# Kernel optimization log

Measured on AMD Instinct MI355X. Metric: run time of the kernel, lower is better.

## Reference

```python
import jax, jax.numpy as jnp
import numpy as np
from jax import lax

B = 2
IMG = 640.0
MIN_LEVEL, MAX_LEVEL = 3, 7
NUM_CLASSES = 91          # includes background (index 0)
MAX_TOTAL = 100
IOU_THR = 0.3
SCORE_THR = 0.05
PRE_NMS = 5000
BBOX_CLIP = float(np.log(1000.0 / 16.0))  # standard box-transform clip


def _level_anchors(level):
    """RetinaNet-style anchors for one pyramid level, [H*W*9, 4] in (y1,x1,y2,x2)."""
    stride = 2 ** level
    feat = int(IMG) // stride
    cy = (np.arange(feat, dtype=np.float32) + 0.5) * stride
    cx = (np.arange(feat, dtype=np.float32) + 0.5) * stride
    cy, cx = np.meshgrid(cy, cx, indexing='ij')
    base = 4.0 * stride
    anchors = []
    for octave in (2 ** 0.0, 2 ** (1.0 / 3.0), 2 ** (2.0 / 3.0)):
        for ar in (0.5, 1.0, 2.0):
            h = base * octave * np.sqrt(ar)
            w = base * octave / np.sqrt(ar)
            anchors.append(np.stack([cy - h / 2, cx - w / 2, cy + h / 2, cx + w / 2], -1))
    a = np.stack(anchors, -2).reshape(-1, 4)
    return a.astype(np.float32)


def setup_inputs():
    key = jax.random.key(0)
    inp = {}
    for level in range(MIN_LEVEL, MAX_LEVEL + 1):
        anc = _level_anchors(level)
        n = anc.shape[0]
        key, kb, kc = jax.random.split(key, 3)
        inp[f'box_outputs_{level}'] = 0.2 * jax.random.normal(kb, (B, n, 4), jnp.float32)
        inp[f'class_outputs_{level}'] = jax.random.normal(kc, (B, n, NUM_CLASSES), jnp.float32) - 2.0
        inp[f'anchor_boxes_{level}'] = jnp.broadcast_to(jnp.asarray(anc)[None], (B, n, 4))
    inp['image_shape'] = jnp.full((B, 2), IMG, jnp.float32)
    return inp


def _decode_boxes(enc, anchors):
    # faithful to box_utils.decode_boxes (with the +1/-1 pixel convention)
    dy, dx = enc[..., 0], enc[..., 1]
    dh = jnp.minimum(enc[..., 2], BBOX_CLIP)
    dw = jnp.minimum(enc[..., 3], BBOX_CLIP)
    ah = anchors[..., 2] - anchors[..., 0] + 1.0
    aw = anchors[..., 3] - anchors[..., 1] + 1.0
    ayc = anchors[..., 0] + 0.5 * ah
    axc = anchors[..., 1] + 0.5 * aw
    yc = dy * ah + ayc
    xc = dx * aw + axc
    h = jnp.exp(dh) * ah
    w = jnp.exp(dw) * aw
    ymin = yc - 0.5 * h
    xmin = xc - 0.5 * w
    return jnp.stack([ymin, xmin, ymin + h - 1.0, xmin + w - 1.0], axis=-1)


def _clip_boxes(boxes, image_shape):
    h = image_shape[:, 0:1]
    w = image_shape[:, 1:2]
    max_len = jnp.stack([h, w, h, w], axis=-1)  # [B,1,4]
    return jnp.clip(boxes, 0.0, max_len)


def _greedy_nms(scores, boxes):
    """Sorted greedy NMS over one (batch, class) lane.
    scores: [K] sorted descending (filtered entries are -1), boxes: [K,4].
    Returns top MAX_TOTAL selected (score, box) in descending score order,
    padded with score=-1 / zero boxes (matches sorted_non_max_suppression_padded).
    """
    areas = (boxes[:, 2] - boxes[:, 0]) * (boxes[:, 3] - boxes[:, 1])

    def step(active, _):
        masked = jnp.where(active, scores, -jnp.inf)
        i = jnp.argmax(masked)
        s = masked[i]
        valid = s > -1.0
        b = boxes[i]
        yy1 = jnp.maximum(b[0], boxes[:, 0])
        xx1 = jnp.maximum(b[1], boxes[:, 1])
        yy2 = jnp.minimum(b[2], boxes[:, 2])
        xx2 = jnp.minimum(b[3], boxes[:, 3])
        inter = jnp.maximum(yy2 - yy1, 0.0) * jnp.maximum(xx2 - xx1, 0.0)
        iou = inter / ((b[2] - b[0]) * (b[3] - b[1]) + areas - inter + 1e-8)
        active = active & (iou <= IOU_THR)
        active = active.at[i].set(False)
        out_s = jnp.where(valid, s, -1.0)
        out_b = jnp.where(valid, b, jnp.zeros_like(b))
        return active, (out_s, out_b)

    _, (sel_s, sel_b) = lax.scan(step, jnp.ones(scores.shape[0], bool), None, length=MAX_TOTAL)
    return sel_s, sel_b


def reference(box_outputs_3, box_outputs_4, box_outputs_5, box_outputs_6, box_outputs_7,
              class_outputs_3, class_outputs_4, class_outputs_5, class_outputs_6, class_outputs_7,
              anchor_boxes_3, anchor_boxes_4, anchor_boxes_5, anchor_boxes_6, anchor_boxes_7,
              image_shape):
    box_list = [box_outputs_3, box_outputs_4, box_outputs_5, box_outputs_6, box_outputs_7]
    cls_list = [class_outputs_3, class_outputs_4, class_outputs_5, class_outputs_6, class_outputs_7]
    anc_list = [anchor_boxes_3, anchor_boxes_4, anchor_boxes_5, anchor_boxes_6, anchor_boxes_7]

    boxes, scores = [], []
    for bo, co, an in zip(box_list, cls_list, anc_list):
        scores.append(jax.nn.sigmoid(co)[..., 1:])            # drop background class 0
        boxes.append(_clip_boxes(_decode_boxes(bo, an), image_shape))
    boxes = jnp.concatenate(boxes, axis=1)                     # [B,N,4] class-agnostic
    scores = jnp.concatenate(scores, axis=1)                   # [B,N,C]

    scores_t = jnp.transpose(scores, (0, 2, 1))                # [B,C,N]
    k = min(scores_t.shape[-1], PRE_NMS)
    top_s, idx = lax.top_k(scores_t, k)                        # [B,C,K]
    top_b = jax.vmap(lambda b, i: b[i])(boxes, idx)            # [B,C,K,4]

    # filter_boxes_by_scores: score -> -1, boxes -> 0 below threshold
    mask = top_s >= SCORE_THR
    top_s = jnp.where(mask, top_s, -1.0)
    top_b = top_b * mask[..., None].astype(top_b.dtype)

    sel_s, sel_b = jax.vmap(jax.vmap(_greedy_nms))(top_s, top_b)  # [B,C,T], [B,C,T,4]
    Bsz, C, T = sel_s.shape
    classes = jnp.broadcast_to(jnp.arange(C, dtype=jnp.int32)[None, :, None], (Bsz, C, T))

    flat_s = sel_s.reshape(Bsz, C * T)
    flat_b = sel_b.reshape(Bsz, C * T, 4)
    flat_c = classes.reshape(Bsz, C * T)

    final_s, fidx = lax.top_k(flat_s, MAX_TOTAL)
    final_b = jnp.take_along_axis(flat_b, fidx[..., None], axis=1)
    final_c = jnp.take_along_axis(flat_c, fidx, axis=1) + 1    # nmsed_classes += 1
    valid = jnp.sum((final_s > -1.0).astype(jnp.int32), axis=1)
    return final_b, final_s, final_c, valid
```

## Files before the change

kernel.cpp:

```cpp
#include <hip/hip_runtime.h>
#include <hip/hip_bf16.h>

typedef unsigned long long u64;
typedef unsigned int u32;

#define A_TOTAL 76725
#define NCLS 90
#define KTOP 5000u
#define MAXT 100
#define KTHR 0x3D4CCCCDu
#define TCAP 2048u
#define SCAP 512u
#define NSEL 384u

__device__ __forceinline__ u64 pack_key(u32 k, u32 i) {
  return ((u64)k << 32) | (u64)(0xFFFFFFFFu - i);
}

__device__ __forceinline__ int dig05(u64 k) {
  float s = __uint_as_float((u32)(k >> 32));
  int d = (int)((s - 0.5f) * 8175.0f);
  return min(max(d, 0), 4095);
}

__device__ __forceinline__ void cut4096w(const u32* hh, u32 need, int wl,
                                         u32& B, u32& incl, u32& above, u32& total) {
  int lo = wl << 6;
  u32 s = 0;
  #pragma unroll
  for (int j = 0; j < 64; ++j) s += hh[lo + j];
  u32 suf = s;
  #pragma unroll
  for (int off = 1; off < 64; off <<= 1) {
    u32 v = __shfl_down(suf, off, 64);
    if (wl < 64 - off) suf += v;
  }
  total = __shfl(suf, 0, 64);
  if (total < need) { B = 0; incl = total; above = 0; return; }
  u32 sufnext = suf - s;
  bool cross = (suf >= need) && (sufnext < need);
  u64 bal = __ballot(cross);
  int gl = (int)__ffsll((unsigned long long)bal) - 1;
  int glo = gl << 6;
  u32 aboveG = __shfl(sufnext, gl, 64);
  u32 hb = hh[glo + wl];
  u32 sufb = hb;
  #pragma unroll
  for (int off = 1; off < 64; off <<= 1) {
    u32 v = __shfl_down(sufb, off, 64);
    if (wl < 64 - off) sufb += v;
  }
  bool c2 = (aboveG + sufb >= need) && (aboveG + sufb - hb < need);
  u64 bal2 = __ballot(c2);
  int jB = (int)__ffsll((unsigned long long)bal2) - 1;
  B = (u32)(glo + jB);
  incl = aboveG + __shfl(sufb, jB, 64);
  above = incl - __shfl(hb, jB, 64);
}

__device__ __forceinline__ void bitonic_desc(u64* a, u32 n, int tid, int nth) {
  u32 P = 2; while (P < n) P <<= 1;
  for (u32 i = tid; i < P; i += nth) if (i >= n) a[i] = 0ULL;
  __syncthreads();
  for (u32 kk = 2; kk <= P; kk <<= 1) {
    for (u32 jj = kk >> 1; jj; jj >>= 1) {
      for (u32 i = tid; i < P; i += nth) {
        u32 ixj = i ^ jj;
        if (ixj > i) {
          u64 x = a[i], y = a[ixj];
          bool up = ((i & kk) == 0);
          if (up ? (x < y) : (x > y)) { a[i] = y; a[ixj] = x; }
        }
      }
      __syncthreads();
    }
  }
}

__device__ __forceinline__ int lazy_scan_g(const u64* key_s, const float4* boxes4, size_t bbase,
                                           int C, float4* wbox, float* outS, float* outB,
                                           int w, int wl) {
  int cur = 0;
  while (w < MAXT && cur < C) {
    int p = cur + wl;
    bool alive = (p < C);
    u64 kk = alive ? key_s[p] : 0ull;
    float4 mybox = make_float4(0.f, 0.f, 0.f, 0.f);
    if (alive) {
      u32 idx = 0xFFFFFFFFu - (u32)(kk & 0xFFFFFFFFull);
      mybox = boxes4[bbase + idx];
    }
    float myarea = alive ? (mybox.z - mybox.x) * (mybox.w - mybox.y) : 0.f;
    for (int j = 0; j < w; ++j) {
      if (alive) {
        float4 pb = wbox[j];
        float yy1 = fmaxf(pb.x, mybox.x), xx1 = fmaxf(pb.y, mybox.y);
        float yy2 = fminf(pb.z, mybox.z), xx2 = fminf(pb.w, mybox.w);
        float inter = fmaxf(yy2 - yy1, 0.0f) * fmaxf(xx2 - xx1, 0.0f);
        if (inter > 0.0f) {
          float pa = (pb.z - pb.x) * (pb.w - pb.y);
          if (inter / (pa + myarea - inter + 1e-8f) > 0.3f) alive = false;
        }
      }
    }
    for (;;) {
      u64 bal = __ballot(alive);
      if (bal == 0ull) break;
      int js = (int)__ffsll((unsigned long long)bal) - 1;
      float4 pb;
      pb.x = __shfl(mybox.x, js, 64);
      pb.y = __shfl(mybox.y, js, 64);
      pb.z = __shfl(mybox.z, js, 64);
      pb.w = __shfl(mybox.w, js, 64);
      u64 wk = __shfl(kk, js, 64);
      if (wl == 0) {
        outS[w] = __uint_as_float((u32)(wk >> 32));
        *(float4*)(outB + w * 4) = pb;
        wbox[w] = pb;
      }
      w++;
      if (w >= MAXT) break;
      if (wl <= js) alive = false;
      else if (alive) {
        float yy1 = fmaxf(pb.x, mybox.x), xx1 = fmaxf(pb.y, mybox.y);
        float yy2 = fminf(pb.z, mybox.z), xx2 = fminf(pb.w, mybox.w);
        float inter = fmaxf(yy2 - yy1, 0.0f) * fmaxf(xx2 - xx1, 0.0f);
        if (inter > 0.0f) {
          float pa = (pb.z - pb.x) * (pb.w - pb.y);
          if (inter / (pa + myarea - inter + 1e-8f) > 0.3f) alive = false;
        }
      }
    }
    cur += 64;
  }
  return w;
}

__device__ __forceinline__ void coll_elem(int i, float x, int b, int base, int slice,
                                          u64* __restrict__ listT_g, u32* __restrict__ cnt_pad) {
  if (x >= 0.0f) {
    u32 a = (u32)i / 91u;
    u32 c = (u32)i - a * 91u;
    if (c != 0u) {
      float s = 1.0f / (1.0f + expf(-x));
      int lane = b * NCLS + (int)c - 1;
      u32 idx = (u32)base + a;
      u32 p = atomicAdd(&cnt_pad[lane * 128 + slice * 16], 1u);
      if (p < SCAP) listT_g[(((size_t)lane * 8 + slice) << 9) + p] = pack_key(__float_as_uint(s), idx);
    }
  }
}

__global__ __launch_bounds__(256) void front_kernel(
    const float* __restrict__ bx0, const float* __restrict__ bx1, const float* __restrict__ bx2,
    const float* __restrict__ bx3, const float* __restrict__ bx4,
    const float* __restrict__ an0, const float* __restrict__ an1, const float* __restrict__ an2,
    const float* __restrict__ an3, const float* __restrict__ an4,
    const float* __restrict__ c3, const float* __restrict__ c4, const float* __restrict__ c5,
    const float* __restrict__ c6, const float* __restrict__ c7,
    const float* __restrict__ img, float* __restrict__ boxes,
    u64* __restrict__ listT_g, u32* __restrict__ cnt_pad)
{
  int blk = blockIdx.x, tid = threadIdx.x;
  if (blk < 600) {
    int t = blk * 256 + tid;
    if (t >= 2 * A_TOTAL) return;
    int b = t / A_TOTAL, a = t % A_TOTAL;
    const float* bp; const float* ap; int al; int nl;
    if (a < 57600)      { bp = bx0; ap = an0; al = a;          nl = 57600; }
    else if (a < 72000) { bp = bx1; ap = an1; al = a - 57600;  nl = 14400; }
    else if (a < 75600) { bp = bx2; ap = an2; al = a - 72000;  nl = 3600;  }
    else if (a < 76500) { bp = bx3; ap = an3; al = a - 75600;  nl = 900;   }
    else                { bp = bx4; ap = an4; al = a - 76500;  nl = 225;   }
    float4 e  = *(const float4*)(bp + ((size_t)b * nl + al) * 4);
    float4 an = *(const float4*)(ap + ((size_t)b * nl + al) * 4);
    const float CLIP = 4.135166556742356f;
    float ah  = an.z - an.x + 1.0f;
    float aw  = an.w - an.y + 1.0f;
    float ayc = an.x + 0.5f * ah;
    float axc = an.y + 0.5f * aw;
    float dh = fminf(e.z, CLIP), dw = fminf(e.w, CLIP);
    float yc = e.x * ah + ayc;
    float xc = e.y * aw + axc;
    float h  = expf(dh) * ah;
    float w  = expf(dw) * aw;
    float ymin = yc - 0.5f * h;
    float xmin = xc - 0.5f * w;
    float ymax = ymin + h - 1.0f;
    float xmax = xmin + w - 1.0f;
    float H = img[b * 2 + 0], W = img[b * 2 + 1];
    float4 o;
    o.x = fminf(fmaxf(ymin, 0.0f), H);
    o.y = fminf(fmaxf(xmin, 0.0f), W);
    o.z = fminf(fmaxf(ymax, 0.0f), H);
    o.w = fminf(fmaxf(xmax, 0.0f), W);
    *(float4*)(boxes + (size_t)t * 4) = o;
    return;
  }
  int blk2 = blk - 600;
  int slice = blk2 & 7;
  const float* cls; int n, base, b, loc, J, lvl;
  if (blk2 < 2560)      { lvl = 0; cls = c3; n = 57600; base = 0;     J = 1280; int r = blk2;        b = r >= J; loc = b ? r - J : r; }
  else if (blk2 < 3200) { lvl = 1; cls = c4; n = 14400; base = 57600; J = 320;  int r = blk2 - 2560; b = r >= J; loc = b ? r - J : r; }
  else if (blk2 < 3360) { lvl = 2; cls = c5; n = 3600;  base = 72000; J = 80;   int r = blk2 - 3200; b = r >= J; loc = b ? r - J : r; }
  else if (blk2 < 3400) { lvl = 3; cls = c6; n = 900;   base = 75600; J = 20;   int r = blk2 - 3360; b = r >= J; loc = b ? r - J : r; }
  else                  { lvl = 4; cls = c7; n = 225;   base = 76500; J = 10;   int r = blk2 - 3400; b = r >= J; loc = b ? r - J : r; }

  if (lvl <= 3) {
    int F4 = n * 91 / 4;
    int chunk = (F4 + J - 1) / J;
    int q0 = loc * chunk;
    int q1 = q0 + chunk; if (q1 > F4) q1 = F4;
    const float4* src4 = (const float4*)(cls + (size_t)b * n * 91);
    for (int q = q0 + tid; q < q1; q += 256) {
      float4 v = src4[q];
      int i0 = q << 2;
      coll_elem(i0,     v.x, b, base, slice, listT_g, cnt_pad);
      coll_elem(i0 + 1, v.y, b, base, slice, listT_g, cnt_pad);
      coll_elem(i0 + 2, v.z, b, base, slice, listT_g, cnt_pad);
      coll_elem(i0 + 3, v.w, b, base, slice, listT_g, cnt_pad);
    }
  } else {
    int F = n * 91;
    int chunk = (F + J - 1) / J;
    int s0 = loc * chunk;
    int s1 = s0 + chunk; if (s1 > F) s1 = F;
    const float* src = cls + (size_t)b * F;
    for (int i = s0 + tid; i < s1; i += 256) coll_elem(i, src[i], b, base, slice, listT_g, cnt_pad);
  }
}

__global__ __launch_bounds__(256) void nms_kernel(
    const float* __restrict__ c3, const float* __restrict__ c4, const float* __restrict__ c5,
    const float* __restrict__ c6, const float* __restrict__ c7,
    const float* __restrict__ boxes, const u64* __restrict__ listT_g,
    const u32* __restrict__ cnt_pad, float* __restrict__ nms_s, float* __restrict__ nms_b)
{
  __shared__ __align__(16) char big[40960];
  __shared__ __align__(16) u64 listE[2048];
  __shared__ u64 key_s[2048];
  __shared__ __align__(16) u32 histL[4096];
  __shared__ float4 wbox[MAXT];
  __shared__ u32 wtot[4];
  __shared__ u32 sh_flag, sh_mid, sh_bigS, sh_cS;
  __shared__ u64 sh_minPrev;
  __shared__ u32 sh_w, sh_done, sh_eidx, sh_Rthr, sh_eSorted, sh_bigF;
  __shared__ u32 sh_B, sh_incl, sh_above, sh_total, sh_cA, sh_cE, sh_B2;

  int tid = threadIdx.x;
  int lane = blockIdx.x;
  int b = lane / NCLS, c = lane % NCLS;
  const float4* boxes4 = (const float4*)boxes;
  size_t bbase = (size_t)b * A_TOTAL;
  const u64 thrpack = ((u64)KTHR) << 32;

  float* outS = nms_s + (size_t)lane * MAXT;
  float* outB = nms_b + (size_t)lane * MAXT * 4;

  u32 pre[9]; pre[0] = 0;
  bool of = false;
  #pragma unroll
  for (int j = 0; j < 8; ++j) {
    u32 cj = cnt_pad[lane * 128 + j * 16];
    of |= (cj > SCAP);
    pre[j + 1] = pre[j] + cj;
  }
  u32 cnt = pre[8];
  if (tid == 0) { sh_flag = (of || cnt > TCAP) ? 1u : 0u; sh_mid = 0; sh_bigS = 0; }
  __syncthreads();

  if (!sh_flag) {
    u64 kr[8];
    #pragma unroll
    for (int r = 0; r < 8; ++r) {
      u32 s = (u32)tid + (u32)r * 256u;
      u64 k = 0ull;
      if (s < cnt) {
        u32 j = 0;
        #pragma unroll
        for (int t = 1; t < 8; ++t) if (s >= pre[t]) j = (u32)t;
        k = listT_g[(((size_t)lane * 8 + j) << 9) + (s - pre[j])];
      }
      kr[r] = k;
    }

    for (int i = tid; i < 4096; i += 256) histL[i] = 0;
    __syncthreads();
    #pragma unroll
    for (int r = 0; r < 8; ++r) if (kr[r]) atomicAdd(&histL[dig05(kr[r])], 1u);
    __syncthreads();
    if (tid < 64) {
      u32 Bx, ix, ax, tx;
      cut4096w(histL, NSEL, tid, Bx, ix, ax, tx);
      if (tid == 0) { sh_B = Bx; sh_incl = ix; sh_total = tx; sh_cS = 0; }
    }
    __syncthreads();
    u32 B = sh_B, incl = sh_incl, total = sh_total;
    bool selAll = (total < NSEL);
    u32 Csel = selAll ? total : incl;
    if (Csel <= 768u) {
      u64* sel = (u64*)histL;
      #pragma unroll
      for (int r = 0; r < 8; ++r) {
        u64 k = kr[r];
        if (k && (selAll || (u32)dig05(k) >= B)) {
          u32 p = atomicAdd(&sh_cS, 1u);
          if (p < 768u) sel[p] = k;
        }
      }
      __syncthreads();
      u32 Cs = sh_cS; if (Cs > 768u) Cs = 768u;
      for (u32 j = tid; j < Cs; j += 256) {
        u64 kj = sel[j];
        u32 rk = 0;
        for (u32 i2 = 0; i2 < Cs; ++i2) rk += (sel[i2] > kj) ? 1u : 0u;
        key_s[rk] = kj;
      }
      __syncthreads();
      if (tid < 64) {
        int w = lazy_scan_g(key_s, boxes4, bbase, (int)Cs, wbox, outS, outB, 0, tid);
        if (tid == 0) {
          sh_w = (u32)w;
          if (w < MAXT) { if (selAll) sh_flag = 1; else sh_mid = 1; }
        }
      }
    } else {
      if (tid == 0) sh_mid = 1;
    }
    __syncthreads();

    if (sh_mid && !sh_flag) {
      for (int i = tid; i < 4096; i += 256) histL[i] = 0;
      if (tid == 0) sh_bigS = 0;
      __syncthreads();
      #pragma unroll
      for (int r = 0; r < 8; ++r) if (kr[r]) atomicAdd(&histL[dig05(kr[r])], 1u);
      __syncthreads();
      {
        int t0 = tid << 4;
        u32 hloc[16]; u32 ssum = 0;
        #pragma unroll
        for (int j = 0; j < 16; ++j) { hloc[j] = histL[t0 + j]; ssum += hloc[j]; }
        int wl = tid & 63, wid = tid >> 6;
        u32 suf = ssum;
        #pragma unroll
        for (int off = 1; off < 64; off <<= 1) {
          u32 v = __shfl_down(suf, off, 64);
          if (wl < 64 - off) suf += v;
        }
        if (wl == 0) wtot[wid] = suf;
        __syncthreads();
        u32 cross = 0;
        for (int w2 = wid + 1; w2 < 4; ++w2) cross += wtot[w2];
        u32 run = (suf - ssum) + cross;
        #pragma unroll
        for (int j = 15; j >= 0; --j) { u32 b2 = run; run += hloc[j]; histL[t0 + j] = b2; }
      }
      __syncthreads();
      #pragma unroll
      for (int r = 0; r < 8; ++r) {
        u64 k = kr[r];
        if (k) {
          u32 pos = atomicAdd(&histL[dig05(k)], 1u);
          if (pos < TCAP) key_s[pos] = k;
        }
      }
      __syncthreads();
      {
        int t0 = tid << 4;
        for (int j = 0; j < 16; ++j) {
          u32 d = (u32)(t0 + j);
          u32 end = histL[d];
          u32 start = (d == 4095u) ? 0u : histL[d + 1];
          u32 cc = end - start;
          if (cc >= 2u) {
            if (cc <= 48u) {
              for (u32 a2 = start + 1; a2 < end; ++a2) {
                u64 kv = key_s[a2];
                int bi = (int)a2 - 1;
                while (bi >= (int)start && key_s[bi] < kv) { key_s[bi + 1] = key_s[bi]; --bi; }
                key_s[bi + 1] = kv;
              }
            } else sh_bigS = 1;
          }
        }
      }
      __syncthreads();
      if (sh_bigS) bitonic_desc(key_s, cnt, tid, 256);
      if (tid < 64) {
        int w = lazy_scan_g(key_s, boxes4, bbase, (int)cnt, wbox, outS, outB, 0, tid);
        if (tid == 0) {
          sh_w = (u32)w;
          if (w < MAXT) sh_flag = 1;
        }
      }
    }
  }
  __syncthreads();
  if (!sh_flag) {
    u32 w = sh_w;
    for (u32 p = w + (u32)tid; p < MAXT; p += 256) {
      outS[p] = -1.0f;
      *(float4*)(outB + p * 4) = make_float4(0.f, 0.f, 0.f, 0.f);
    }
    return;
  }

  auto sb_of = [&](int i) -> u32 {
    const float* p; int al, nl;
    if (i < 57600)      { p = c3; al = i;          nl = 57600; }
    else if (i < 72000) { p = c4; al = i - 57600;  nl = 14400; }
    else if (i < 75600) { p = c5; al = i - 72000;  nl = 3600;  }
    else if (i < 76500) { p = c6; al = i - 75600;  nl = 900;   }
    else                { p = c7; al = i - 76500;  nl = 225;   }
    float x = p[((size_t)b * nl + al) * 91 + (c + 1)];
    float s = 1.0f / (1.0f + expf(-x));
    return __float_as_uint(s);
  };

  u64* listA = (u64*)big;
  for (int i = tid; i < 4096; i += 256) histL[i] = 0;
  if (tid == 0) {
    sh_cA = 0; sh_cE = 0; sh_w = 0; sh_done = 0; sh_eidx = 0; sh_eSorted = 0; sh_minPrev = ~0ull;
  }
  __syncthreads();
  for (int i = tid; i < A_TOTAL; i += 256) atomicAdd(&histL[sb_of(i) >> 19], 1u);
  __syncthreads();
  if (tid < 64) {
    u32 Bx, ix, ax, tx;
    cut4096w(histL, KTOP, tid, Bx, ix, ax, tx);
    if (tid == 0) sh_B = Bx;
  }
  __syncthreads();
  u32 B = sh_B;
  for (int i = tid; i < A_TOTAL; i += 256) {
    u32 u = sb_of(i);
    u32 bkt = u >> 19;
    if (bkt > B) {
      u32 p = atomicAdd(&sh_cA, 1u);
      if (p < 5120u) listA[p] = pack_key(u, (u32)i);
    } else if (bkt == B) {
      u32 p = atomicAdd(&sh_cE, 1u);
      if (p < 2048u) listE[p] = pack_key(u, (u32)i);
    }
  }
  __syncthreads();
  u32 g = sh_cA, h = sh_cE;
  if (h > 2048u) {
    for (int i = tid; i < 4096; i += 256) histL[i] = 0;
    if (tid == 0) sh_cE = 0;
    __syncthreads();
    for (int i = tid; i < A_TOTAL; i += 256) {
      u32 u = sb_of(i);
      if ((u >> 19) == B) atomicAdd(&histL[(u >> 7) & 0xFFFu], 1u);
    }
    __syncthreads();
    u32 R1 = KTOP - g;
    if (tid < 64) {
      u32 Bx, ix, ax, tx;
      cut4096w(histL, R1, tid, Bx, ix, ax, tx);
      if (tid == 0) sh_B2 = Bx;
    }
    __syncthreads();
    u32 B2 = sh_B2;
    for (int i = tid; i < A_TOTAL; i += 256) {
      u32 u = sb_of(i);
      if ((u >> 19) == B) {
        u32 sb2 = (u >> 7) & 0xFFFu;
        if (sb2 > B2) {
          u32 p = atomicAdd(&sh_cA, 1u);
          if (p < 5120u) listA[p] = pack_key(u, (u32)i);
        } else if (sb2 == B2) {
          u32 p = atomicAdd(&sh_cE, 1u);
          if (p < 2048u) listE[p] = pack_key(u, (u32)i);
        }
      }
    }
    __syncthreads();
    g = sh_cA; h = sh_cE; if (h > 2048u) h = 2048u;
  }
  if (g > 5120u) g = 5120u;
  u32 R = (g < KTOP) ? (KTOP - g) : 0u; if (R > h) R = h;

  u64 ak[20];
  #pragma unroll
  for (int r = 0; r < 20; ++r) {
    u32 s2 = (u32)tid + (u32)r * 256u;
    u64 kp = (s2 < g) ? listA[s2] : 0ull;
    if (kp < thrpack) kp = 0ull;
    ak[r] = kp;
  }
  __syncthreads();
  u32* cntArr = (u32*)big;

  const float LO0  = 0.04f;
  const float INV0 = 4096.0f / (1.001f - 0.04f);

  for (int seg = 0; seg < 7200; ++seg) {
    __syncthreads();
    if (sh_w >= MAXT || sh_done) break;
    u64 minPrev = sh_minPrev;

    int digLvl = 0;
    u32 A_B0 = 0, A_B1 = 0;
    float lo1 = 0.f, inv1 = 0.f;
    u64 kMask = 0, kPref = 0;
    int m1shift = 32;
    int selMode = -1;
    u32 selB = 0;
    u32 C = 0;
    bool fromE = false;

    for (int lvl = 0; lvl < 8; ++lvl) {
      for (int i = tid; i < 4096; i += 256) histL[i] = 0;
      __syncthreads();
      #pragma unroll
      for (int r = 0; r < 20; ++r) {
        u64 k = ak[r];
        if (!k || k >= minPrev) continue;
        float s = __uint_as_float((u32)(k >> 32));
        if (digLvl >= 1) { int d0 = (int)((s - LO0) * INV0); d0 = min(max(d0, 0), 4095); if ((u32)d0 != A_B0) continue; }
        if (digLvl >= 2) { int d1 = (int)((s - lo1) * inv1); d1 = min(max(d1, 0), 4095); if ((u32)d1 != A_B1) continue; }
        if (digLvl >= 3 && ((k & kMask) != kPref)) continue;
        u32 d;
        if (digLvl == 0)      { int t0 = (int)((s - LO0) * INV0); d = (u32)min(max(t0, 0), 4095); }
        else if (digLvl == 1) { int t1 = (int)((s - lo1) * inv1); d = (u32)min(max(t1, 0), 4095); }
        else                  d = (u32)((k >> m1shift) & 0xFFFull);
        atomicAdd(&histL[d], 1u);
      }
      __syncthreads();
      if (tid < 64) {
        u32 Bx, ix, ax, tx;
        cut4096w(histL, 1024u, tid, Bx, ix, ax, tx);
        if (tid == 0) { sh_B = Bx; sh_incl = ix; sh_above = ax; sh_total = tx; }
      }
      __syncthreads();
      u32 total = sh_total, incl = sh_incl, above = sh_above, Bx = sh_B;
      if (total == 0u)   { fromE = true; break; }
      if (total < 1024u) { selMode = 0; C = total; break; }
      if (incl <= 2048u) { selMode = 1; selB = Bx; C = incl; break; }
      if (above > 0u)    { selMode = 2; selB = Bx; C = above; break; }
      if (digLvl == 0) {
        A_B0 = Bx;
        lo1 = LO0 + (float)Bx / INV0;
        inv1 = INV0 * 4096.0f;
        digLvl = 1;
      } else if (digLvl == 1) {
        A_B1 = Bx;
        digLvl = 2; m1shift = 32;
      } else {
        kPref |= ((u64)Bx << m1shift);
        kMask |= (0xFFFull << m1shift);
        m1shift -= 12;
        digLvl++;
      }
      __syncthreads();
    }

    if (fromE) {
      if (!sh_eSorted) {
        bitonic_desc(listE, h, tid, 256);
        if (tid == 0) {
          u32 lo = 0, hi2 = h;
          while (lo < hi2) { u32 mid = (lo + hi2) >> 1; if (listE[mid] >= thrpack) lo = mid + 1; else hi2 = mid; }
          sh_Rthr = (R < lo) ? R : lo;
          sh_eSorted = 1;
        }
        __syncthreads();
      }
      u32 eidx = sh_eidx;
      u32 take = (sh_Rthr > eidx) ? (sh_Rthr - eidx) : 0u;
      if (take > 2048u) take = 2048u;
      if (take == 0u) { if (tid == 0) sh_done = 1; continue; }
      for (u32 i = tid; i < take; i += 256) key_s[i] = listE[eidx + i];
      C = take;
      if (tid == 0) sh_eidx = eidx + take;
    } else {
      u32 hloc[16];
      {
        int t0 = tid << 4;
        u32 ssum = 0;
        #pragma unroll
        for (int j = 0; j < 16; ++j) { hloc[j] = histL[t0 + j]; ssum += hloc[j]; }
        int wl = tid & 63, wid = tid >> 6;
        u32 suf = ssum;
        #pragma unroll
        for (int off = 1; off < 64; off <<= 1) {
          u32 v = __shfl_down(suf, off, 64);
          if (wl < 64 - off) suf += v;
        }
        if (wl == 0) wtot[wid] = suf;
        __syncthreads();
        u32 cross = 0;
        for (int w2 = wid + 1; w2 < 4; ++w2) cross += wtot[w2];
        u32 run = (suf - ssum) + cross;
        #pragma unroll
        for (int j = 15; j >= 0; --j) { u32 base2 = run; run += hloc[j]; histL[t0 + j] = base2; }
      }
      for (int i = tid; i < 4096; i += 256) cntArr[i] = 0;
      if (tid == 0) sh_bigF = 0;
      __syncthreads();
      #pragma unroll
      for (int r = 0; r < 20; ++r) {
        u64 k = ak[r];
        if (!k || k >= minPrev) continue;
        float s = __uint_as_float((u32)(k >> 32));
        if (digLvl >= 1) { int d0 = (int)((s - LO0) * INV0); d0 = min(max(d0, 0), 4095); if ((u32)d0 != A_B0) continue; }
        if (digLvl >= 2) { int d1 = (int)((s - lo1) * inv1); d1 = min(max(d1, 0), 4095); if ((u32)d1 != A_B1) continue; }
        if (digLvl >= 3 && ((k & kMask) != kPref)) continue;
        u32 d;
        if (digLvl == 0)      { int t0x = (int)((s - LO0) * INV0); d = (u32)min(max(t0x, 0), 4095); }
        else if (digLvl == 1) { int t1x = (int)((s - lo1) * inv1); d = (u32)min(max(t1x, 0), 4095); }
        else                  d = (u32)((k >> m1shift) & 0xFFFull);
        if (selMode == 1)      { if (d < selB) continue; }
        else if (selMode == 2) { if (d <= selB) continue; }
        u32 pos = histL[d] + atomicAdd(&cntArr[d], 1u);
        if (pos < 2048u) key_s[pos] = k;
      }
      __syncthreads();
      {
        int t0 = tid << 4;
        for (int j = 0; j < 16; ++j) {
          u32 bkt = (u32)(t0 + j);
          u32 cc = cntArr[bkt];
          if (cc >= 2u) {
            if (cc <= 48u) {
              u32 basep = histL[bkt];
              for (u32 a2 = 1; a2 < cc; ++a2) {
                u64 kv = key_s[basep + a2];
                int bi = (int)a2 - 1;
                while (bi >= 0 && key_s[basep + bi] < kv) { key_s[basep + bi + 1] = key_s[basep + bi]; --bi; }
                key_s[basep + bi + 1] = kv;
              }
            } else sh_bigF = 1;
          }
        }
      }
      __syncthreads();
      if (sh_bigF) bitonic_desc(key_s, C, tid, 256);
      if (tid == 0) sh_minPrev = key_s[C - 1];
    }
    __syncthreads();

    if (tid < 64) {
      int w = lazy_scan_g(key_s, boxes4, bbase, (int)C, wbox, outS, outB, (int)sh_w, tid);
      if (tid == 0) sh_w = (u32)w;
    }
  }

  __syncthreads();
  u32 w = sh_w;
  for (u32 p = w + (u32)tid; p < MAXT; p += 256) {
    outS[p] = -1.0f;
    *(float4*)(outB + p * 4) = make_float4(0.f, 0.f, 0.f, 0.f);
  }
}

__global__ __launch_bounds__(256) void merge_kernel(
    const float* __restrict__ nms_s, const float* __restrict__ nms_b,
    float* __restrict__ out_b, float* __restrict__ out_s,
    float* __restrict__ out_c, float* __restrict__ out_v)
{
  __shared__ u64 keys[NCLS * MAXT];
  __shared__ u32 hist[4096];
  __shared__ u64 sel[640];
  __shared__ u32 sh_cnt, sh_valid;
  __shared__ u32 sh_B, sh_incl, sh_above, sh_total;

  int b = blockIdx.x, tid = threadIdx.x;
  const int NTOT = NCLS * MAXT;

  for (int i = tid; i < NTOT; i += 256) {
    float s = nms_s[(size_t)b * NTOT + i];
    u32 u = __float_as_uint(s);
    u = (u & 0x80000000u) ? ~u : (u | 0x80000000u);
    keys[i] = ((u64)u << 32) | (u64)(0xFFFFFFFFu - (u32)i);
  }
  if (tid == 0) { sh_cnt = 0; sh_valid = 0; }

  u64 prefVal = 0;
  u64 T = 0;
  u32 need = MAXT;
  const int shifts[6] = {52, 40, 28, 16, 4, 0};
  const int widths[6] = {12, 12, 12, 12, 12, 4};
  for (int lvl = 0; lvl < 6; ++lvl) {
    int s = shifts[lvl], w = widths[lvl];
    for (int i = tid; i < 4096; i += 256) hist[i] = 0;
    __syncthreads();
    u32 dmask = (1u << w) - 1u;
    for (int i = tid; i < NTOT; i += 256) {
      u64 k = keys[i];
      if (lvl > 0 && (k >> (s + w)) != (prefVal >> (s + w))) continue;
      atomicAdd(&hist[(u32)((k >> s) & dmask)], 1u);
    }
    __syncthreads();
    if (tid < 64) {
      u32 Bx, ix, ax, tx;
      cut4096w(hist, need, tid, Bx, ix, ax, tx);
      if (tid == 0) { sh_B = Bx; sh_incl = ix; sh_above = ax; sh_total = tx; }
    }
    __syncthreads();
    u32 B = sh_B, incl = sh_incl, above = sh_above;
    if (incl <= 512u || lvl == 5) {
      T = prefVal | ((u64)B << s);
      break;
    }
    prefVal |= ((u64)B << s);
    need -= above;
  }
  __syncthreads();

  for (int i = tid; i < NTOT; i += 256) {
    u64 k = keys[i];
    if (k >= T) {
      u32 p = atomicAdd(&sh_cnt, 1u);
      if (p < 640u) sel[p] = k;
    }
  }
  __syncthreads();
  u32 cnt = sh_cnt; if (cnt > 640u) cnt = 640u;

  for (u32 j = tid; j < cnt; j += 256) {
    u64 kj = sel[j];
    u32 r = 0;
    for (u32 i = 0; i < cnt; ++i) r += (sel[i] > kj) ? 1u : 0u;
    if (r < (u32)MAXT) {
      u32 u = (u32)(kj >> 32);
      u32 bits = (u & 0x80000000u) ? (u ^ 0x80000000u) : ~u;
      float sc = __uint_as_float(bits);
      u32 flat = 0xFFFFFFFFu - (u32)(kj & 0xFFFFFFFFull);
      int cls = (int)(flat / MAXT), pos = (int)(flat % MAXT);
      out_s[b * MAXT + r] = sc;
      out_c[b * MAXT + r] = (float)(cls + 1);
      *(float4*)(out_b + ((size_t)b * MAXT + r) * 4) =
          *(const float4*)(nms_b + (((size_t)b * NCLS + cls) * MAXT + pos) * 4);
      if (sc > -1.0f) atomicAdd(&sh_valid, 1u);
    }
  }
  __syncthreads();
  if (tid == 0) out_v[b] = (float)sh_valid;
}

extern "C" void kernel_launch(void* const* d_in, const int* in_sizes, int n_in,
                              void* d_out, int out_size, void* d_ws, size_t ws_size,
                              hipStream_t stream)
{
  const float* box[5]; const float* cls[5]; const float* anc[5];
  bool interleaved = (in_sizes[1] == 2 * 57600 * 91);
  if (interleaved) {
    for (int l = 0; l < 5; ++l) {
      box[l] = (const float*)d_in[3 * l + 0];
      cls[l] = (const float*)d_in[3 * l + 1];
      anc[l] = (const float*)d_in[3 * l + 2];
    }
  } else {
    for (int l = 0; l < 5; ++l) {
      box[l] = (const float*)d_in[l];
      cls[l] = (const float*)d_in[5 + l];
      anc[l] = (const float*)d_in[10 + l];
    }
  }
  const float* img = (const float*)d_in[15];

  float* ws = (float*)d_ws;
  float* boxes_ws = ws;
  u32*   cnt_pad  = (u32*)(boxes_ws + 613800);
  u64*   listT_g  = (u64*)(cnt_pad + 180 * 128);
  float* nms_s    = (float*)(listT_g + 180 * 8 * 512);
  float* nms_b    = nms_s + 18000;

  hipMemsetAsync(cnt_pad, 0, 180 * 128 * sizeof(u32), stream);

  front_kernel<<<4020, 256, 0, stream>>>(
      box[0], box[1], box[2], box[3], box[4],
      anc[0], anc[1], anc[2], anc[3], anc[4],
      cls[0], cls[1], cls[2], cls[3], cls[4],
      img, boxes_ws, listT_g, cnt_pad);

  nms_kernel<<<180, 256, 0, stream>>>(cls[0], cls[1], cls[2], cls[3], cls[4],
                                      boxes_ws, listT_g, cnt_pad, nms_s, nms_b);

  float* out_b = (float*)d_out;
  float* out_s = out_b + 800;
  float* out_c = out_s + 200;
  float* out_v = out_c + 200;
  merge_kernel<<<2, 256, 0, stream>>>(nms_s, nms_b, out_b, out_s, out_c, out_v);
}
```

Measured before the change: 114.9 us.

## Split monolithic NMS kernel into sort, scan and fallback kernels

The single per-class NMS kernel is split into three launches. A 256-thread sort kernel does a full histogram-bucket sort of the candidate keys into global memory. A 64-thread scan kernel with small shared memory runs the lazy greedy NMS scan, and a fallback kernel handles only the classes flagged as overflowing or short. The partial top-384 selection path is dropped. The broadcast of the winning box now goes through shared memory instead of five shuffles. This is meant to cut the heavy shared-memory footprint and idle threads during the serial scan, at the cost of extra launches and a global round trip for the sorted keys.

```diff
diff --git a/kernel.cpp b/kernel.cpp
--- a/kernel.cpp
+++ b/kernel.cpp
@@ -11,7 +11,6 @@
 #define KTHR 0x3D4CCCCDu
 #define TCAP 2048u
 #define SCAP 512u
-#define NSEL 384u
 
 __device__ __forceinline__ u64 pack_key(u32 k, u32 i) {
   return ((u64)k << 32) | (u64)(0xFFFFFFFFu - i);
@@ -107,17 +106,12 @@
       u64 bal = __ballot(alive);
       if (bal == 0ull) break;
       int js = (int)__ffsll((unsigned long long)bal) - 1;
-      float4 pb;
-      pb.x = __shfl(mybox.x, js, 64);
-      pb.y = __shfl(mybox.y, js, 64);
-      pb.z = __shfl(mybox.z, js, 64);
-      pb.w = __shfl(mybox.w, js, 64);
-      u64 wk = __shfl(kk, js, 64);
-      if (wl == 0) {
-        outS[w] = __uint_as_float((u32)(wk >> 32));
-        *(float4*)(outB + w * 4) = pb;
-        wbox[w] = pb;
-      }
+      if (wl == js) {
+        wbox[w] = mybox;
+        outS[w] = __uint_as_float((u32)(kk >> 32));
+        *(float4*)(outB + w * 4) = mybox;
+      }
+      float4 pb = wbox[w];
       w++;
       if (w >= MAXT) break;
       if (wl <= js) alive = false;
@@ -230,32 +224,16 @@
   }
 }
 
-__global__ __launch_bounds__(256) void nms_kernel(
-    const float* __restrict__ c3, const float* __restrict__ c4, const float* __restrict__ c5,
-    const float* __restrict__ c6, const float* __restrict__ c7,
-    const float* __restrict__ boxes, const u64* __restrict__ listT_g,
-    const u32* __restrict__ cnt_pad, float* __restrict__ nms_s, float* __restrict__ nms_b)
+__global__ __launch_bounds__(256) void sort_kernel(
+    const u64* __restrict__ listT_g, const u32* __restrict__ cnt_pad,
+    u64* __restrict__ sortedK, u32* __restrict__ C_g, u32* __restrict__ flags)
 {
-  __shared__ __align__(16) char big[40960];
-  __shared__ __align__(16) u64 listE[2048];
+  __shared__ u32 histL[4096];
   __shared__ u64 key_s[2048];
-  __shared__ __align__(16) u32 histL[4096];
-  __shared__ float4 wbox[MAXT];
   __shared__ u32 wtot[4];
-  __shared__ u32 sh_flag, sh_mid, sh_bigS, sh_cS;
-  __shared__ u64 sh_minPrev;
-  __shared__ u32 sh_w, sh_done, sh_eidx, sh_Rthr, sh_eSorted, sh_bigF;
-  __shared__ u32 sh_B, sh_incl, sh_above, sh_total, sh_cA, sh_cE, sh_B2;
-
+  __shared__ u32 sh_big;
   int tid = threadIdx.x;
   int lane = blockIdx.x;
-  int b = lane / NCLS, c = lane % NCLS;
-  const float4* boxes4 = (const float4*)boxes;
-  size_t bbase = (size_t)b * A_TOTAL;
-  const u64 thrpack = ((u64)KTHR) << 32;
-
-  float* outS = nms_s + (size_t)lane * MAXT;
-  float* outB = nms_b + (size_t)lane * MAXT * 4;
 
   u32 pre[9]; pre[0] = 0;
   bool of = false;
@@ -266,145 +244,134 @@
     pre[j + 1] = pre[j] + cj;
   }
   u32 cnt = pre[8];
-  if (tid == 0) { sh_flag = (of || cnt > TCAP) ? 1u : 0u; sh_mid = 0; sh_bigS = 0; }
-  __syncthreads();
-
-  if (!sh_flag) {
-    u64 kr[8];
+  if (of || cnt > TCAP) {
+    if (tid == 0) { flags[lane] = 1; C_g[lane] = 0; }
+    return;
+  }
+  if (tid == 0) { C_g[lane] = cnt; sh_big = 0; }
+
+  u64 kr[8];
+  #pragma unroll
+  for (int r = 0; r < 8; ++r) {
+    u32 s = (u32)tid + (u32)r * 256u;
+    u64 k = 0ull;
+    if (s < cnt) {
+      u32 j = 0;
+      #pragma unroll
+      for (int t = 1; t < 8; ++t) if (s >= pre[t]) j = (u32)t;
+      k = listT_g[(((size_t)lane * 8 + j) << 9) + (s - pre[j])];
+    }
+    kr[r] = k;
+  }
+
+  for (int i = tid; i < 4096; i += 256) histL[i] = 0;
+  __syncthreads();
+  #pragma unroll
+  for (int r = 0; r < 8; ++r) if (kr[r]) atomicAdd(&histL[dig05(kr[r])], 1u);
+  __syncthreads();
+  {
+    int t0 = tid << 4;
+    u32 hloc[16]; u32 ssum = 0;
     #pragma unroll
-    for (int r = 0; r < 8; ++r) {
-      u32 s = (u32)tid + (u32)r * 256u;
-      u64 k = 0ull;
-      if (s < cnt) {
-        u32 j = 0;
-        #pragma unroll
-        for (int t = 1; t < 8; ++t) if (s >= pre[t]) j = (u32)t;
-        k = listT_g[(((size_t)lane * 8 + j) << 9) + (s - pre[j])];
-      }
-      kr[r] = k;
-    }
-
-    for (int i = tid; i < 4096; i += 256) histL[i] = 0;
-    __syncthreads();
+    for (int j = 0; j < 16; ++j) { hloc[j] = histL[t0 + j]; ssum += hloc[j]; }
+    int wl = tid & 63, wid = tid >> 6;
+    u32 suf = ssum;
     #pragma unroll
-    for (int r = 0; r < 8; ++r) if (kr[r]) atomicAdd(&histL[dig05(kr[r])], 1u);
-    __syncthreads();
-    if (tid < 64) {
-      u32 Bx, ix, ax, tx;
-      cut4096w(histL, NSEL, tid, Bx, ix, ax, tx);
-      if (tid == 0) { sh_B = Bx; sh_incl = ix; sh_total = tx; sh_cS = 0; }
-    }
-    __syncthreads();
-    u32 B = sh_B, incl = sh_incl, total = sh_total;
-    bool selAll = (total < NSEL);
-    u32 Csel = selAll ? total : incl;
-    if (Csel <= 768u) {
-      u64* sel = (u64*)histL;
-      #pragma unroll
-      for (int r = 0; r < 8; ++r) {
-        u64 k = kr[r];
-        if (k && (selAll || (u32)dig05(k) >= B)) {
-          u32 p = atomicAdd(&sh_cS, 1u);
-          if (p < 768u) sel[p] = k;
-        }
-      }
-      __syncthreads();
-      u32 Cs = sh_cS; if (Cs > 768u) Cs = 768u;
-      for (u32 j = tid; j < Cs; j += 256) {
-        u64 kj = sel[j];
-        u32 rk = 0;
-        for (u32 i2 = 0; i2 < Cs; ++i2) rk += (sel[i2] > kj) ? 1u : 0u;
-        key_s[rk] = kj;
-      }
-      __syncthreads();
-      if (tid < 64) {
-        int w = lazy_scan_g(key_s, boxes4, bbase, (int)Cs, wbox, outS, outB, 0, tid);
-        if (tid == 0) {
-          sh_w = (u32)w;
-          if (w < MAXT) { if (selAll) sh_flag = 1; else sh_mid = 1; }
-        }
-      }
-    } else {
-      if (tid == 0) sh_mid = 1;
-    }
-    __syncthreads();
-
-    if (sh_mid && !sh_flag) {
-      for (int i = tid; i < 4096; i += 256) histL[i] = 0;
-      if (tid == 0) sh_bigS = 0;
-      __syncthreads();
-      #pragma unroll
-      for (int r = 0; r < 8; ++r) if (kr[r]) atomicAdd(&histL[dig05(kr[r])], 1u);
-      __syncthreads();
-      {
-        int t0 = tid << 4;
-        u32 hloc[16]; u32 ssum = 0;
-        #pragma unroll
-        for (int j = 0; j < 16; ++j) { hloc[j] = histL[t0 + j]; ssum += hloc[j]; }
-        int wl = tid & 63, wid = tid >> 6;
-        u32 suf = ssum;
-        #pragma unroll
-        for (int off = 1; off < 64; off <<= 1) {
-          u32 v = __shfl_down(suf, off, 64);
-          if (wl < 64 - off) suf += v;
-        }
-        if (wl == 0) wtot[wid] = suf;
-        __syncthreads();
-        u32 cross = 0;
-        for (int w2 = wid + 1; w2 < 4; ++w2) cross += wtot[w2];
-        u32 run = (suf - ssum) + cross;
-        #pragma unroll
-        for (int j = 15; j >= 0; --j) { u32 b2 = run; run += hloc[j]; histL[t0 + j] = b2; }
-      }
-      __syncthreads();
-      #pragma unroll
-      for (int r = 0; r < 8; ++r) {
-        u64 k = kr[r];
-        if (k) {
-          u32 pos = atomicAdd(&histL[dig05(k)], 1u);
-          if (pos < TCAP) key_s[pos] = k;
-        }
-      }
-      __syncthreads();
-      {
-        int t0 = tid << 4;
-        for (int j = 0; j < 16; ++j) {
-          u32 d = (u32)(t0 + j);
-          u32 end = histL[d];
-          u32 start = (d == 4095u) ? 0u : histL[d + 1];
-          u32 cc = end - start;
-          if (cc >= 2u) {
-            if (cc <= 48u) {
-              for (u32 a2 = start + 1; a2 < end; ++a2) {
-                u64 kv = key_s[a2];
-                int bi = (int)a2 - 1;
-                while (bi >= (int)start && key_s[bi] < kv) { key_s[bi + 1] = key_s[bi]; --bi; }
-                key_s[bi + 1] = kv;
-              }
-            } else sh_bigS = 1;
+    for (int off = 1; off < 64; off <<= 1) {
+      u32 v = __shfl_down(suf, off, 64);
+      if (wl < 64 - off) suf += v;
+    }
+    if (wl == 0) wtot[wid] = suf;
+    __syncthreads();
+    u32 cross = 0;
+    for (int w2 = wid + 1; w2 < 4; ++w2) cross += wtot[w2];
+    u32 run = (suf - ssum) + cross;
+    #pragma unroll
+    for (int j = 15; j >= 0; --j) { u32 b2 = run; run += hloc[j]; histL[t0 + j] = b2; }
+  }
+  __syncthreads();
+  #pragma unroll
+  for (int r = 0; r < 8; ++r) {
+    u64 k = kr[r];
+    if (k) {
+      u32 pos = atomicAdd(&histL[dig05(k)], 1u);
+      if (pos < TCAP) key_s[pos] = k;
+    }
+  }
+  __syncthreads();
+  {
+    int t0 = tid << 4;
+    for (int j = 0; j < 16; ++j) {
+      u32 d = (u32)(t0 + j);
+      u32 end = histL[d];
+      u32 start = (d == 4095u) ? 0u : histL[d + 1];
+      u32 cc = end - start;
+      if (cc >= 2u) {
+        if (cc <= 48u) {
+          for (u32 a2 = start + 1; a2 < end; ++a2) {
+            u64 kv = key_s[a2];
+            int bi = (int)a2 - 1;
+            while (bi >= (int)start && key_s[bi] < kv) { key_s[bi + 1] = key_s[bi]; --bi; }
+            key_s[bi + 1] = kv;
           }
-        }
-      }
-      __syncthreads();
-      if (sh_bigS) bitonic_desc(key_s, cnt, tid, 256);
-      if (tid < 64) {
-        int w = lazy_scan_g(key_s, boxes4, bbase, (int)cnt, wbox, outS, outB, 0, tid);
-        if (tid == 0) {
-          sh_w = (u32)w;
-          if (w < MAXT) sh_flag = 1;
-        }
-      }
-    }
-  }
-  __syncthreads();
-  if (!sh_flag) {
-    u32 w = sh_w;
-    for (u32 p = w + (u32)tid; p < MAXT; p += 256) {
-      outS[p] = -1.0f;
-      *(float4*)(outB + p * 4) = make_float4(0.f, 0.f, 0.f, 0.f);
-    }
-    return;
-  }
+        } else sh_big = 1;
+      }
+    }
+  }
+  __syncthreads();
+  if (sh_big) bitonic_desc(key_s, cnt, tid, 256);
+  u64* SK = sortedK + (size_t)lane * TCAP;
+  for (u32 p = tid; p < cnt; p += 256) SK[p] = key_s[p];
+}
+
+__global__ __launch_bounds__(64) void scan_kernel(
+    const u64* __restrict__ sortedK, const float* __restrict__ boxes,
+    const u32* __restrict__ C_g, u32* __restrict__ flags,
+    float* __restrict__ nms_s, float* __restrict__ nms_b)
+{
+  __shared__ u64 key_s[TCAP];
+  __shared__ float4 wbox[MAXT];
+  int lane = blockIdx.x;
+  int wl = threadIdx.x;
+  if (flags[lane]) return;
+  int C = (int)C_g[lane];
+  const u64* SK = sortedK + (size_t)lane * TCAP;
+  for (int i = wl; i < C; i += 64) key_s[i] = SK[i];
+  __builtin_amdgcn_s_waitcnt(0);
+  const float4* boxes4 = (const float4*)boxes;
+  size_t bbase = (size_t)(lane / NCLS) * A_TOTAL;
+  float* outS = nms_s + (size_t)lane * MAXT;
+  float* outB = nms_b + (size_t)lane * MAXT * 4;
+  int w = lazy_scan_g(key_s, boxes4, bbase, C, wbox, outS, outB, 0, wl);
+  if (w < MAXT) { if (wl == 0) flags[lane] = 1; return; }
+}
+
+__global__ __launch_bounds__(256) void fb_kernel(
+    const float* __restrict__ c3, const float* __restrict__ c4, const float* __restrict__ c5,
+    const float* __restrict__ c6, const float* __restrict__ c7,
+    const float* __restrict__ boxes, const u32* __restrict__ flags,
+    float* __restrict__ nms_s, float* __restrict__ nms_b)
+{
+  __shared__ __align__(16) char big[40960];
+  __shared__ __align__(16) u64 listE[2048];
+  __shared__ u64 key_s[2048];
+  __shared__ u32 histL[4096];
+  __shared__ float4 wbox[MAXT];
+  __shared__ u32 wtot[4];
+  __shared__ u64 sh_minPrev;
+  __shared__ u32 sh_w, sh_done, sh_eidx, sh_Rthr, sh_eSorted, sh_bigF;
+  __shared__ u32 sh_B, sh_incl, sh_above, sh_total, sh_cA, sh_cE, sh_B2;
+
+  int lane = blockIdx.x;
+  if (flags[lane] == 0) return;
+  int tid = threadIdx.x;
+  int b = lane / NCLS, c = lane % NCLS;
+  const float4* boxes4 = (const float4*)boxes;
+  size_t bbase = (size_t)b * A_TOTAL;
+  const u64 thrpack = ((u64)KTHR) << 32;
+
+  float* outS = nms_s + (size_t)lane * MAXT;
+  float* outB = nms_b + (size_t)lane * MAXT * 4;
 
   auto sb_of = [&](int i) -> u32 {
     const float* p; int al, nl;
@@ -765,11 +732,14 @@
   float* ws = (float*)d_ws;
   float* boxes_ws = ws;
   u32*   cnt_pad  = (u32*)(boxes_ws + 613800);
-  u64*   listT_g  = (u64*)(cnt_pad + 180 * 128);
-  float* nms_s    = (float*)(listT_g + 180 * 8 * 512);
+  u32*   flags    = cnt_pad + 180 * 128;
+  u32*   C_g      = flags + 180;
+  u64*   listT_g  = (u64*)(C_g + 180 + 2);
+  u64*   sortedK  = listT_g + 180 * 8 * 512;
+  float* nms_s    = (float*)(sortedK + 180 * 2048);
   float* nms_b    = nms_s + 18000;
 
-  hipMemsetAsync(cnt_pad, 0, 180 * 128 * sizeof(u32), stream);
+  hipMemsetAsync(cnt_pad, 0, (180 * 128 + 360) * sizeof(u32), stream);
 
   front_kernel<<<4020, 256, 0, stream>>>(
       box[0], box[1], box[2], box[3], box[4],
@@ -777,8 +747,12 @@
       cls[0], cls[1], cls[2], cls[3], cls[4],
       img, boxes_ws, listT_g, cnt_pad);
 
-  nms_kernel<<<180, 256, 0, stream>>>(cls[0], cls[1], cls[2], cls[3], cls[4],
-                                      boxes_ws, listT_g, cnt_pad, nms_s, nms_b);
+  sort_kernel<<<180, 256, 0, stream>>>(listT_g, cnt_pad, sortedK, C_g, flags);
+
+  scan_kernel<<<180, 64, 0, stream>>>(sortedK, boxes_ws, C_g, flags, nms_s, nms_b);
+
+  fb_kernel<<<180, 256, 0, stream>>>(cls[0], cls[1], cls[2], cls[3], cls[4],
+                                     boxes_ws, flags, nms_s, nms_b);
 
   float* out_b = (float*)d_out;
   float* out_s = out_b + 800;
```

Result: slower. 136.6 us (+18.9%).

## Replace serial shuffle NMS scan with per-chunk IoU bitmask suppression

Applied to the files above, without the earlier changes.

Adds a bitset-based greedy NMS scan. Each lane of a 64-wide chunk precomputes a 64-bit mask of the chunk candidates it suppresses, and the greedy pick loop then just clears bits, replacing the per-winner shuffle-and-recompute IoU loop. Both scan paths also drop the alive guard in the loop over earlier winners so it runs without branching. The hipMemsetAsync is replaced by a small zero kernel to cut launch/memset overhead. The trade-off is always doing 64 IoU tests per lane per chunk, even when few winners are picked.

```diff
diff --git a/kernel.cpp b/kernel.cpp
--- a/kernel.cpp
+++ b/kernel.cpp
@@ -77,6 +77,71 @@
   }
 }
 
+__device__ __forceinline__ int bitset_scan(const u64* key_s, const float4* boxes4, size_t bbase,
+                                           int C, float4* wbox, float4* bbox,
+                                           float* outS, float* outB, int w, int wl) {
+  int cur = 0;
+  while (w < MAXT && cur < C) {
+    int p = cur + wl;
+    bool valid = (p < C);
+    u64 kk = valid ? key_s[p] : 0ull;
+    float4 mybox = make_float4(-3e30f, -3e30f, -3e30f, -3e30f);
+    if (valid) {
+      u32 idx = 0xFFFFFFFFu - (u32)(kk & 0xFFFFFFFFull);
+      mybox = boxes4[bbase + idx];
+    }
+    bbox[wl] = mybox;
+    float myarea = (mybox.z - mybox.x) * (mybox.w - mybox.y);
+    bool alive = valid;
+    for (int j = 0; j < w; ++j) {
+      float4 pb = wbox[j];
+      float yy1 = fmaxf(pb.x, mybox.x), xx1 = fmaxf(pb.y, mybox.y);
+      float yy2 = fminf(pb.z, mybox.z), xx2 = fminf(pb.w, mybox.w);
+      float inter = fmaxf(yy2 - yy1, 0.0f) * fmaxf(xx2 - xx1, 0.0f);
+      bool bad = false;
+      if (inter > 0.0f) {
+        float pa = (pb.z - pb.x) * (pb.w - pb.y);
+        bad = inter / (pa + myarea - inter + 1e-8f) > 0.3f;
+      }
+      alive = alive && !bad;
+    }
+    u64 krow = 0ull;
+    int jmax = C - cur; if (jmax > 64) jmax = 64;
+    for (int j = 0; j < jmax; ++j) {
+      float4 pb = bbox[j];
+      float yy1 = fmaxf(pb.x, mybox.x), xx1 = fmaxf(pb.y, mybox.y);
+      float yy2 = fminf(pb.z, mybox.z), xx2 = fminf(pb.w, mybox.w);
+      float inter = fmaxf(yy2 - yy1, 0.0f) * fmaxf(xx2 - xx1, 0.0f);
+      bool kill = false;
+      if (inter > 0.0f) {
+        float pa = (pb.z - pb.x) * (pb.w - pb.y);
+        kill = inter / (pa + myarea - inter + 1e-8f) > 0.3f;
+      }
+      if (kill) krow |= (1ull << j);
+    }
+    u32 krlo = (u32)krow, krhi = (u32)(krow >> 32);
+    u64 amask = __ballot(alive);
+    int myord = -1;
+    while (amask != 0ull && w < MAXT) {
+      int js = (int)__ffsll((unsigned long long)amask) - 1;
+      u32 klo = __shfl(krlo, js, 64);
+      u32 khi = __shfl(krhi, js, 64);
+      u64 kr = ((u64)khi << 32) | (u64)klo;
+      if (wl == js) myord = w;
+      amask &= ~kr;
+      amask &= ~(1ull << js);
+      w++;
+    }
+    if (myord >= 0) {
+      outS[myord] = __uint_as_float((u32)(kk >> 32));
+      *(float4*)(outB + myord * 4) = mybox;
+      wbox[myord] = mybox;
+    }
+    cur += 64;
+  }
+  return w;
+}
+
 __device__ __forceinline__ int lazy_scan_g(const u64* key_s, const float4* boxes4, size_t bbase,
                                            int C, float4* wbox, float* outS, float* outB,
                                            int w, int wl) {
@@ -90,18 +155,18 @@
       u32 idx = 0xFFFFFFFFu - (u32)(kk & 0xFFFFFFFFull);
       mybox = boxes4[bbase + idx];
     }
-    float myarea = alive ? (mybox.z - mybox.x) * (mybox.w - mybox.y) : 0.f;
+    float myarea = (mybox.z - mybox.x) * (mybox.w - mybox.y);
     for (int j = 0; j < w; ++j) {
-      if (alive) {
-        float4 pb = wbox[j];
-        float yy1 = fmaxf(pb.x, mybox.x), xx1 = fmaxf(pb.y, mybox.y);
-        float yy2 = fminf(pb.z, mybox.z), xx2 = fminf(pb.w, mybox.w);
-        float inter = fmaxf(yy2 - yy1, 0.0f) * fmaxf(xx2 - xx1, 0.0f);
-        if (inter > 0.0f) {
-          float pa = (pb.z - pb.x) * (pb.w - pb.y);
-          if (inter / (pa + myarea - inter + 1e-8f) > 0.3f) alive = false;
-        }
-      }
+      float4 pb = wbox[j];
+      float yy1 = fmaxf(pb.x, mybox.x), xx1 = fmaxf(pb.y, mybox.y);
+      float yy2 = fminf(pb.z, mybox.z), xx2 = fminf(pb.w, mybox.w);
+      float inter = fmaxf(yy2 - yy1, 0.0f) * fmaxf(xx2 - xx1, 0.0f);
+      bool bad = false;
+      if (inter > 0.0f) {
+        float pa = (pb.z - pb.x) * (pb.w - pb.y);
+        bad = inter / (pa + myarea - inter + 1e-8f) > 0.3f;
+      }
+      alive = alive && !bad;
     }
     for (;;) {
       u64 bal = __ballot(alive);
@@ -134,6 +199,11 @@
     cur += 64;
   }
   return w;
+}
+
+__global__ __launch_bounds__(256) void zero_kernel(u32* __restrict__ p, int n) {
+  int i = blockIdx.x * 256 + threadIdx.x;
+  if (i < n) p[i] = 0;
 }
 
 __device__ __forceinline__ void coll_elem(int i, float x, int b, int base, int slice,
@@ -241,6 +311,7 @@
   __shared__ u64 key_s[2048];
   __shared__ __align__(16) u32 histL[4096];
   __shared__ float4 wbox[MAXT];
+  __shared__ float4 bbox[64];
   __shared__ u32 wtot[4];
   __shared__ u32 sh_flag, sh_mid, sh_bigS, sh_cS;
   __shared__ u64 sh_minPrev;
@@ -318,7 +389,7 @@
       }
       __syncthreads();
       if (tid < 64) {
-        int w = lazy_scan_g(key_s, boxes4, bbase, (int)Cs, wbox, outS, outB, 0, tid);
+        int w = bitset_scan(key_s, boxes4, bbase, (int)Cs, wbox, bbox, outS, outB, 0, tid);
         if (tid == 0) {
           sh_w = (u32)w;
           if (w < MAXT) { if (selAll) sh_flag = 1; else sh_mid = 1; }
@@ -388,7 +459,7 @@
       __syncthreads();
       if (sh_bigS) bitonic_desc(key_s, cnt, tid, 256);
       if (tid < 64) {
-        int w = lazy_scan_g(key_s, boxes4, bbase, (int)cnt, wbox, outS, outB, 0, tid);
+        int w = bitset_scan(key_s, boxes4, bbase, (int)cnt, wbox, bbox, outS, outB, 0, tid);
         if (tid == 0) {
           sh_w = (u32)w;
           if (w < MAXT) sh_flag = 1;
@@ -769,7 +840,8 @@
   float* nms_s    = (float*)(listT_g + 180 * 8 * 512);
   float* nms_b    = nms_s + 18000;
 
-  hipMemsetAsync(cnt_pad, 0, 180 * 128 * sizeof(u32), stream);
+  const int NZ = 180 * 128;
+  zero_kernel<<<(NZ + 255) / 256, 256, 0, stream>>>(cnt_pad, NZ);
 
   front_kernel<<<4020, 256, 0, stream>>>(
       box[0], box[1], box[2], box[3], box[4],
```

After: 117.9 us. 2.6% more time.
